# Optimization experiments

Measured on AMD Instinct MI355X. Metric: run time of the kernel, lower is better.

Reference implementation:

```python
import jax, jax.numpy as jnp
import numpy as np
import math

B, L, D, H, FF = 8, 1024, 1024, 16, 4096
DT = D // H  # d_tensor per head
EPS = 1e-12


def _layernorm(x, gamma, beta):
    # Faithful: unbiased std (ddof=1), divide by (std + eps)
    mean = jnp.mean(x, axis=-1, keepdims=True)
    std = jnp.std(x, axis=-1, keepdims=True, ddof=1)
    return gamma * ((x - mean) / (std + EPS)) + beta


def setup_inputs() -> dict:
    key = jax.random.key(0)
    ks = jax.random.split(key, 16)
    sc = 1.0 / math.sqrt(D)
    inp = {
        "x": jax.random.normal(ks[0], (B, L, D), jnp.float32),
        "s_mask": jnp.ones((B, 1, L, L), jnp.int32),
        "wq": jax.random.normal(ks[1], (D, D), jnp.float32) * sc,
        "bq": jnp.zeros((D,), jnp.float32),
        "wk": jax.random.normal(ks[2], (D, D), jnp.float32) * sc,
        "bk": jnp.zeros((D,), jnp.float32),
        "wv": jax.random.normal(ks[3], (D, D), jnp.float32) * sc,
        "bv": jnp.zeros((D,), jnp.float32),
        "wc": jax.random.normal(ks[4], (D, D), jnp.float32) * sc,
        "bc": jnp.zeros((D,), jnp.float32),
        "g1": jnp.ones((D,), jnp.float32),
        "be1": jnp.zeros((D,), jnp.float32),
        "w1": jax.random.normal(ks[5], (D, FF), jnp.float32) * sc,
        "b1": jnp.zeros((FF,), jnp.float32),
        "w2": jax.random.normal(ks[6], (FF, D), jnp.float32) / math.sqrt(FF),
        "b2": jnp.zeros((D,), jnp.float32),
        "g2": jnp.ones((D,), jnp.float32),
        "be2": jnp.zeros((D,), jnp.float32),
    }
    return inp


def reference(x, s_mask, wq, bq, wk, bk, wv, bv, wc, bc, g1, be1, w1, b1, w2, b2, g2, be2):
    _x = x
    q = x @ wq + bq
    k = x @ wk + bk
    v = x @ wv + bv
    # Faithful quirk: split() is a VIEW/reshape [B,L,D] -> [B,H,L,DT], not a transpose-based head split.
    q = q.reshape(B, H, L, DT)
    k = k.reshape(B, H, L, DT)
    v = v.reshape(B, H, L, DT)
    # Faithful quirk: k_t is a reshape to [B,H,DT,L], not a transpose.
    k_t = k.reshape(B, H, DT, L)
    score = jnp.einsum('bhld,bhdm->bhlm', q, k_t) / math.sqrt(DT)
    # Faithful quirk: masked_fill value is -1e-12 (not -inf)
    score = jnp.where(s_mask == 0, jnp.float32(-EPS), score)
    # Faithful quirk: nn.Softmax() with dim=None on 4D tensor -> softmax over dim=1 (head axis)
    score = jax.nn.softmax(score, axis=1)
    out = jnp.einsum('bhlm,bhmd->bhld', score, v)
    out = out.reshape(B, L, D)
    out = out @ wc + bc
    x = _layernorm(out + _x, g1, be1)
    # dropout1: identity at inference
    _x = x
    h = jax.nn.relu(x @ w1 + b1)  # FFN dropout also identity at inference
    h = h @ w2 + b2
    x = _layernorm(h + _x, g2, be2)
    return x
```

## Files before the change

### kernel.cpp

```cpp
#include <hip/hip_runtime.h>
#include <stdint.h>

typedef unsigned short u16;
typedef __attribute__((ext_vector_type(8))) short sx8;
typedef __attribute__((ext_vector_type(4))) float fx4;

__device__ __forceinline__ float bf2f(u16 u) {
    union { unsigned i; float f; } v; v.i = ((unsigned)u) << 16; return v.f;
}
__device__ __forceinline__ u16 f2bf(float f) {
    union { float f; unsigned i; } v; v.f = f;
    return (u16)((v.i + 0x7FFFu + ((v.i >> 16) & 1u)) >> 16);
}
#define MFMA(a, b, c) __builtin_amdgcn_mfma_f32_16x16x32_bf16((a), (b), (c), 0, 0, 0)

#define GLDS(gp, lp) \
    __builtin_amdgcn_global_load_lds((const __attribute__((address_space(1))) void*)(gp), \
                                     (__attribute__((address_space(3))) void*)(lp), 16, 0, 0)

template<int BN>
__global__ __launch_bounds__(256) void gemm_bt(
    const u16* __restrict__ A, long sA, int ldA,
    const u16* __restrict__ BT, long sBT, int ldBT,
    u16* __restrict__ C, long sC, int ldC,
    int K,
    const u16* __restrict__ bias, int bz,
    const void* __restrict__ resid, int residF32, long rofs,
    float scale, int relu)
{
    constexpr int BK = 32;
    constexpr int TM = 4;
    constexpr int TN = BN / 32;
    constexpr int AI = 2;
    constexpr int BI = BN / 64;

    __shared__ __align__(16) u16 As[128 * BK];
    __shared__ __align__(16) u16 Bs[BN * BK];

    const int tid  = threadIdx.x;
    const int w    = tid >> 6;
    const int lane = tid & 63;
    const int quad = lane >> 4;
    const int n16  = lane & 15;
    const int wrow = w >> 1, wcol = w & 1;
    const int m0 = blockIdx.y * 128, n0 = blockIdx.x * BN;
    const long z = blockIdx.z;
    A  += z * sA;
    BT += z * sBT;
    C  += z * sC;

    fx4 acc[TM][TN] = {};

    for (int k0 = 0; k0 < K; k0 += BK) {
        #pragma unroll
        for (int i = 0; i < AI; ++i) {
            unsigned base = (unsigned)(w * AI + i) * 1024u;
            unsigned off  = base + (unsigned)lane * 16u;
            unsigned row  = off >> 6;
            unsigned col  = (off & 63u) >> 1;
            GLDS(A + (long)(m0 + row) * ldA + k0 + col, (char*)As + base);
        }
        #pragma unroll
        for (int i = 0; i < BI; ++i) {
            unsigned base = (unsigned)(w * BI + i) * 1024u;
            unsigned off  = base + (unsigned)lane * 16u;
            unsigned row  = off >> 6;
            unsigned col  = (off & 63u) >> 1;
            GLDS(BT + (long)(n0 + row) * ldBT + k0 + col, (char*)Bs + base);
        }
        __syncthreads();

        sx8 af[TM], bfr[TN];
        #pragma unroll
        for (int r = 0; r < TM; ++r)
            af[r] = *(const sx8*)&As[(wrow * 64 + r * 16 + n16) * BK + quad * 8];
        #pragma unroll
        for (int c = 0; c < TN; ++c)
            bfr[c] = *(const sx8*)&Bs[(wcol * (TN * 16) + c * 16 + n16) * BK + quad * 8];
        #pragma unroll
        for (int r = 0; r < TM; ++r)
            #pragma unroll
            for (int c = 0; c < TN; ++c)
                acc[r][c] = MFMA(af[r], bfr[c], acc[r][c]);
        __syncthreads();
    }

    #pragma unroll
    for (int r = 0; r < TM; ++r) {
        int row = m0 + wrow * 64 + r * 16 + quad * 4;
        #pragma unroll
        for (int c = 0; c < TN; ++c) {
            int col = n0 + wcol * (TN * 16) + c * 16 + n16;
            float bv = bias ? bf2f(bias[bz * (int)z + col]) : 0.f;
            #pragma unroll
            for (int g = 0; g < 4; ++g) {
                long idx = (long)(row + g) * ldC + col;
                float xv = acc[r][c][g] * scale + bv;
                if (resid)
                    xv += residF32 ? ((const float*)resid)[rofs + idx]
                                   : bf2f(((const u16*)resid)[rofs + idx]);
                if (relu) xv = fmaxf(xv, 0.f);
                C[idx] = f2bf(xv);
            }
        }
    }
}

__global__ __launch_bounds__(256, 2) void attn_fused(
    const u16* __restrict__ qb, const u16* __restrict__ kt,
    const u16* __restrict__ vt, const int* __restrict__ mask,
    u16* __restrict__ ao)
{
    constexpr int LM = 136;
    constexpr int SH = 16 * LM;
    __shared__ u16 Ss[16 * SH];

    const int tid = threadIdx.x, w = tid >> 6, lane = tid & 63;
    const int quad = lane >> 4, n16 = lane & 15;
    const int l0 = blockIdx.x * 16;
    const long bo = (long)blockIdx.y * 1048576;

    sx8 qf[4][2];
    #pragma unroll
    for (int i = 0; i < 4; ++i) {
        const u16* qp = qb + bo + (w * 4 + i) * 65536 + (l0 + n16) * 64 + quad * 8;
        qf[i][0] = *(const sx8*)qp;
        qf[i][1] = *(const sx8*)(qp + 32);
    }

    fx4 of[4][4] = {};

    for (int mt = 0; mt < 8; ++mt) {
        const int m0 = mt * 128;
        #pragma unroll
        for (int i = 0; i < 4; ++i) {
            const int h = w * 4 + i;
            const u16* kp = kt + bo + h * 65536 + (long)m0 * 64;
            #pragma unroll
            for (int nt = 0; nt < 8; ++nt) {
                const u16* kr = kp + (nt * 16 + n16) * 64 + quad * 8;
                fx4 s = {};
                s = MFMA(qf[i][0], *(const sx8*)kr, s);
                s = MFMA(qf[i][1], *(const sx8*)(kr + 32), s);
                #pragma unroll
                for (int r = 0; r < 4; ++r)
                    Ss[h * SH + (quad * 4 + r) * LM + nt * 16 + n16] = f2bf(s[r] * 0.125f);
            }
        }
        __syncthreads();
        #pragma unroll
        for (int j = 0; j < 4; ++j) {
            const int p = tid + 256 * j;
            const int l = p >> 6, mp = (p & 63) * 2;
            const int2 mk = *(const int2*)&mask[bo + (long)(l0 + l) * 1024 + m0 + mp];
            u16* col = &Ss[l * LM + mp];
            float v0[16], v1[16], mx0 = -1e30f, mx1 = -1e30f;
            #pragma unroll
            for (int h = 0; h < 16; ++h) {
                unsigned pr = *(const unsigned*)&col[h * SH];
                float a = (mk.x == 0) ? -1e-12f : bf2f((u16)(pr & 0xffff));
                float b = (mk.y == 0) ? -1e-12f : bf2f((u16)(pr >> 16));
                v0[h] = a; v1[h] = b;
                mx0 = fmaxf(mx0, a); mx1 = fmaxf(mx1, b);
            }
            float s0 = 0.f, s1 = 0.f;
            #pragma unroll
            for (int h = 0; h < 16; ++h) {
                v0[h] = __expf(v0[h] - mx0); s0 += v0[h];
                v1[h] = __expf(v1[h] - mx1); s1 += v1[h];
            }
            const float i0 = 1.f / s0, i1 = 1.f / s1;
            #pragma unroll
            for (int h = 0; h < 16; ++h)
                *(unsigned*)&col[h * SH] =
                    (unsigned)f2bf(v0[h] * i0) | ((unsigned)f2bf(v1[h] * i1) << 16);
        }
        __syncthreads();
        #pragma unroll
        for (int i = 0; i < 4; ++i) {
            const int h = w * 4 + i;
            const u16* sp = &Ss[h * SH + n16 * LM];
            sx8 af[4];
            #pragma unroll
            for (int ks = 0; ks < 4; ++ks)
                af[ks] = *(const sx8*)(sp + ks * 32 + quad * 8);
            const u16* vp = vt + bo + h * 65536 + (long)n16 * 1024 + m0 + quad * 8;
            #pragma unroll
            for (int dt = 0; dt < 4; ++dt)
                #pragma unroll
                for (int ks = 0; ks < 4; ++ks)
                    of[i][dt] = MFMA(af[ks], *(const sx8*)(vp + dt * 16384 + ks * 32), of[i][dt]);
        }
        __syncthreads();
    }

    #pragma unroll
    for (int i = 0; i < 4; ++i) {
        const int h = w * 4 + i;
        #pragma unroll
        for (int dt = 0; dt < 4; ++dt)
            #pragma unroll
            for (int r = 0; r < 4; ++r)
                ao[bo + h * 65536 + (long)(l0 + quad * 4 + r) * 64 + dt * 16 + n16]
                    = f2bf(of[i][dt][r]);
    }
}

__global__ __launch_bounds__(256) void convert_f2b(
    const float* __restrict__ in, u16* __restrict__ out)
{
    long i = ((long)blockIdx.x * 256 + threadIdx.x) * 4;
    fx4 v = *(const fx4*)(in + i);
    uint2 o;
    o.x = (unsigned)f2bf(v[0]) | ((unsigned)f2bf(v[1]) << 16);
    o.y = (unsigned)f2bf(v[2]) | ((unsigned)f2bf(v[3]) << 16);
    *(uint2*)(out + i) = o;
}

__global__ __launch_bounds__(256) void transpose_f2b(
    const float* __restrict__ in, u16* __restrict__ out, int R, int C)
{
    __shared__ float t[32][33];
    int c0 = blockIdx.x * 32, r0 = blockIdx.y * 32;
    int tx = threadIdx.x & 31, ty = threadIdx.x >> 5;
    #pragma unroll
    for (int i = 0; i < 4; ++i)
        t[ty + i * 8][tx] = in[(long)(r0 + ty + i * 8) * C + c0 + tx];
    __syncthreads();
    #pragma unroll
    for (int i = 0; i < 4; ++i)
        out[(long)(c0 + ty + i * 8) * R + r0 + tx] = f2bf(t[tx][ty + i * 8]);
}

__global__ __launch_bounds__(256) void transpose_bf(
    const u16* __restrict__ in, u16* __restrict__ out, int R, int C)
{
    __shared__ u16 t[32][33];
    long zoff = (long)blockIdx.z * (long)R * (long)C;
    in += zoff; out += zoff;
    int c0 = blockIdx.x * 32, r0 = blockIdx.y * 32;
    int tx = threadIdx.x & 31, ty = threadIdx.x >> 5;
    #pragma unroll
    for (int i = 0; i < 4; ++i)
        t[ty + i * 8][tx] = in[(long)(r0 + ty + i * 8) * C + c0 + tx];
    __syncthreads();
    #pragma unroll
    for (int i = 0; i < 4; ++i)
        out[(long)(c0 + ty + i * 8) * R + r0 + tx] = t[tx][ty + i * 8];
}

__global__ __launch_bounds__(256) void pack_bias(
    const float* bq, const float* bk, const float* bv, const float* bc,
    const float* b1, const float* b2, u16* __restrict__ out)
{
    int i = blockIdx.x * 256 + threadIdx.x;
    float v;
    if      (i < 1024) v = bq[i];
    else if (i < 2048) v = bk[i - 1024];
    else if (i < 3072) v = bv[i - 2048];
    else if (i < 4096) v = bc[i - 3072];
    else if (i < 8192) v = b1[i - 4096];
    else               v = b2[i - 8192];
    out[i] = f2bf(v);
}

__global__ __launch_bounds__(256) void layernorm_row(
    const u16* __restrict__ in, const float* __restrict__ g,
    const float* __restrict__ be, void* __restrict__ out, int outF32)
{
    int wave = threadIdx.x >> 6, lane = threadIdx.x & 63;
    long row = (long)blockIdx.x * 4 + wave;
    const u16* p = in + row * 1024 + lane * 16;

    float x[16];
    uint4 a = ((const uint4*)p)[0], b = ((const uint4*)p)[1];
    {
        unsigned u;
        u = a.x; x[0] = bf2f(u & 0xffff);  x[1] = bf2f(u >> 16);
        u = a.y; x[2] = bf2f(u & 0xffff);  x[3] = bf2f(u >> 16);
        u = a.z; x[4] = bf2f(u & 0xffff);  x[5] = bf2f(u >> 16);
        u = a.w; x[6] = bf2f(u & 0xffff);  x[7] = bf2f(u >> 16);
        u = b.x; x[8] = bf2f(u & 0xffff);  x[9] = bf2f(u >> 16);
        u = b.y; x[10] = bf2f(u & 0xffff); x[11] = bf2f(u >> 16);
        u = b.z; x[12] = bf2f(u & 0xffff); x[13] = bf2f(u >> 16);
        u = b.w; x[14] = bf2f(u & 0xffff); x[15] = bf2f(u >> 16);
    }
    float s = 0.f, ss = 0.f;
    #pragma unroll
    for (int i = 0; i < 16; ++i) { s += x[i]; ss += x[i] * x[i]; }
    #pragma unroll
    for (int o = 32; o >= 1; o >>= 1) { s += __shfl_down(s, o); ss += __shfl_down(ss, o); }
    s = __shfl(s, 0); ss = __shfl(ss, 0);
    float mean = s * (1.f / 1024.f);
    float var  = fmaxf((ss - 1024.f * mean * mean) * (1.f / 1023.f), 0.f);
    float rinv = 1.f / (sqrtf(var) + 1e-12f);

    int col = lane * 16;
    if (outF32) {
        float* ov = (float*)out + row * 1024 + col;
        #pragma unroll
        for (int i = 0; i < 16; ++i)
            ov[i] = g[col + i] * ((x[i] - mean) * rinv) + be[col + i];
    } else {
        u16* ov = (u16*)out + row * 1024 + col;
        #pragma unroll
        for (int i = 0; i < 16; ++i)
            ov[i] = f2bf(g[col + i] * ((x[i] - mean) * rinv) + be[col + i]);
    }
}

extern "C" void kernel_launch(void* const* d_in, const int* in_sizes, int n_in,
                              void* d_out, int out_size, void* d_ws, size_t ws_size,
                              hipStream_t stream)
{
    const float* xf  = (const float*)d_in[0];
    const int* mask  = (const int*)d_in[1];
    const float* wq = (const float*)d_in[2];  const float* bq = (const float*)d_in[3];
    const float* wk = (const float*)d_in[4];  const float* bk = (const float*)d_in[5];
    const float* wv = (const float*)d_in[6];  const float* bv = (const float*)d_in[7];
    const float* wc = (const float*)d_in[8];  const float* bc = (const float*)d_in[9];
    const float* g1 = (const float*)d_in[10]; const float* be1 = (const float*)d_in[11];
    const float* w1 = (const float*)d_in[12]; const float* b1 = (const float*)d_in[13];
    const float* w2 = (const float*)d_in[14]; const float* b2 = (const float*)d_in[15];
    const float* g2 = (const float*)d_in[16]; const float* be2 = (const float*)d_in[17];

    char* ws = (char*)d_ws;
    const long MB = 1 << 20;
    u16* xb    = (u16*)(ws + 0 * MB);
    u16* wqkvT = (u16*)(ws + 16 * MB);
    u16* wcT   = (u16*)(ws + 22 * MB);
    u16* qb    = (u16*)(ws + 24 * MB);
    u16* kb    = (u16*)(ws + 40 * MB);
    u16* vb    = (u16*)(ws + 56 * MB);
    u16* kt    = (u16*)(ws + 72 * MB);
    u16* vt    = (u16*)(ws + 40 * MB);
    u16* biasp = (u16*)(ws + 96 * MB);
    u16* ao   = xb;
    u16* t0   = qb;
    u16* fh   = kb;
    u16* w1T  = (u16*)(ws + 72 * MB);
    u16* w2T  = (u16*)(ws + 80 * MB);
    u16* pre2 = (u16*)(ws + 88 * MB);

    dim3 blk(256);
    const long M1 = 1048576;

    convert_f2b<<<dim3(8192), blk, 0, stream>>>(xf, xb);
    transpose_f2b<<<dim3(32, 32), blk, 0, stream>>>(wq, wqkvT, 1024, 1024);
    transpose_f2b<<<dim3(32, 32), blk, 0, stream>>>(wk, wqkvT + M1, 1024, 1024);
    transpose_f2b<<<dim3(32, 32), blk, 0, stream>>>(wv, wqkvT + 2 * M1, 1024, 1024);
    transpose_f2b<<<dim3(32, 32), blk, 0, stream>>>(wc, wcT, 1024, 1024);
    pack_bias<<<dim3(36), blk, 0, stream>>>(bq, bk, bv, bc, b1, b2, biasp);

    gemm_bt<128><<<dim3(8, 64, 3), blk, 0, stream>>>(
        xb, 0, 1024, wqkvT, M1, 1024, qb, 8 * M1, 1024, 1024,
        biasp, 1024, nullptr, 0, 0, 1.f, 0);

    transpose_bf<<<dim3(32, 2, 128), blk, 0, stream>>>(kb, kt, 64, 1024);

    transpose_bf<<<dim3(2, 32, 128), blk, 0, stream>>>(vb, vt, 1024, 64);
    attn_fused<<<dim3(64, 8), blk, 0, stream>>>(qb, kt, vt, mask, ao);

    gemm_bt<128><<<dim3(8, 64, 1), blk, 0, stream>>>(
        ao, 0, 1024, wcT, 0, 1024, t0, 0, 1024, 1024,
        biasp + 3072, 0, xf, 1, 0, 1.f, 0);
    layernorm_row<<<dim3(2048), blk, 0, stream>>>(t0, g1, be1, t0, 0);

    transpose_f2b<<<dim3(128, 32), blk, 0, stream>>>(w1, w1T, 1024, 4096);
    transpose_f2b<<<dim3(32, 128), blk, 0, stream>>>(w2, w2T, 4096, 1024);

    for (int c = 0; c < 2; ++c) {
        long r0 = (long)c * 4096 * 1024;
        gemm_bt<128><<<dim3(32, 32, 1), blk, 0, stream>>>(
            t0 + r0, 0, 1024, w1T, 0, 1024, fh, 0, 4096, 1024,
            biasp + 4096, 0, nullptr, 0, 0, 1.f, 1);
        gemm_bt<64><<<dim3(16, 32, 1), blk, 0, stream>>>(
            fh, 0, 4096, w2T, 0, 4096, pre2, 0, 1024, 4096,
            biasp + 8192, 0, t0 + r0, 0, 0, 1.f, 0);
        layernorm_row<<<dim3(1024), blk, 0, stream>>>(
            pre2, g2, be2, (float*)d_out + r0, 1);
    }
}
```

Measured before the change: 956.4 us.

## Split attention key range across two blocks and sum partial outputs

```diff
diff --git a/kernel.cpp b/kernel.cpp
--- a/kernel.cpp
+++ b/kernel.cpp
@@ -106,19 +106,22 @@
     }
 }
 
-__global__ __launch_bounds__(256, 2) void attn_fused(
+__global__ __launch_bounds__(256, 4) void attn_fused(
     const u16* __restrict__ qb, const u16* __restrict__ kt,
     const u16* __restrict__ vt, const int* __restrict__ mask,
-    u16* __restrict__ ao)
-{
-    constexpr int LM = 136;
+    u16* __restrict__ p0, u16* __restrict__ p1)
+{
+    constexpr int MC = 64;
+    constexpr int LM = MC + 8;
     constexpr int SH = 16 * LM;
-    __shared__ u16 Ss[16 * SH];
+    __shared__ __align__(16) u16 Ss[16 * SH];
 
     const int tid = threadIdx.x, w = tid >> 6, lane = tid & 63;
     const int quad = lane >> 4, n16 = lane & 15;
     const int l0 = blockIdx.x * 16;
     const long bo = (long)blockIdx.y * 1048576;
+    const int mbase = blockIdx.z * 512;
+    u16* __restrict__ po = blockIdx.z ? p1 : p0;
 
     sx8 qf[4][2];
     #pragma unroll
@@ -131,27 +134,28 @@
     fx4 of[4][4] = {};
 
     for (int mt = 0; mt < 8; ++mt) {
-        const int m0 = mt * 128;
+        const int m0 = mbase + mt * MC;
         #pragma unroll
         for (int i = 0; i < 4; ++i) {
             const int h = w * 4 + i;
             const u16* kp = kt + bo + h * 65536 + (long)m0 * 64;
             #pragma unroll
-            for (int nt = 0; nt < 8; ++nt) {
+            for (int nt = 0; nt < 4; ++nt) {
                 const u16* kr = kp + (nt * 16 + n16) * 64 + quad * 8;
                 fx4 s = {};
-                s = MFMA(qf[i][0], *(const sx8*)kr, s);
-                s = MFMA(qf[i][1], *(const sx8*)(kr + 32), s);
-                #pragma unroll
-                for (int r = 0; r < 4; ++r)
-                    Ss[h * SH + (quad * 4 + r) * LM + nt * 16 + n16] = f2bf(s[r] * 0.125f);
+                s = MFMA(*(const sx8*)kr,        qf[i][0], s);
+                s = MFMA(*(const sx8*)(kr + 32), qf[i][1], s);
+                uint2 pk;
+                pk.x = (unsigned)f2bf(s[0] * 0.125f) | ((unsigned)f2bf(s[1] * 0.125f) << 16);
+                pk.y = (unsigned)f2bf(s[2] * 0.125f) | ((unsigned)f2bf(s[3] * 0.125f) << 16);
+                *(uint2*)&Ss[h * SH + n16 * LM + nt * 16 + quad * 4] = pk;
             }
         }
         __syncthreads();
         #pragma unroll
-        for (int j = 0; j < 4; ++j) {
+        for (int j = 0; j < 2; ++j) {
             const int p = tid + 256 * j;
-            const int l = p >> 6, mp = (p & 63) * 2;
+            const int l = p >> 5, mp = (p & 31) * 2;
             const int2 mk = *(const int2*)&mask[bo + (long)(l0 + l) * 1024 + m0 + mp];
             u16* col = &Ss[l * LM + mp];
             float v0[16], v1[16], mx0 = -1e30f, mx1 = -1e30f;
@@ -180,16 +184,14 @@
         for (int i = 0; i < 4; ++i) {
             const int h = w * 4 + i;
             const u16* sp = &Ss[h * SH + n16 * LM];
-            sx8 af[4];
-            #pragma unroll
-            for (int ks = 0; ks < 4; ++ks)
-                af[ks] = *(const sx8*)(sp + ks * 32 + quad * 8);
+            sx8 a0 = *(const sx8*)(sp + quad * 8);
+            sx8 a1 = *(const sx8*)(sp + 32 + quad * 8);
             const u16* vp = vt + bo + h * 65536 + (long)n16 * 1024 + m0 + quad * 8;
             #pragma unroll
-            for (int dt = 0; dt < 4; ++dt)
-                #pragma unroll
-                for (int ks = 0; ks < 4; ++ks)
-                    of[i][dt] = MFMA(af[ks], *(const sx8*)(vp + dt * 16384 + ks * 32), of[i][dt]);
+            for (int dt = 0; dt < 4; ++dt) {
+                of[i][dt] = MFMA(a0, *(const sx8*)(vp + dt * 16384),      of[i][dt]);
+                of[i][dt] = MFMA(a1, *(const sx8*)(vp + dt * 16384 + 32), of[i][dt]);
+            }
         }
         __syncthreads();
     }
@@ -201,9 +203,26 @@
         for (int dt = 0; dt < 4; ++dt)
             #pragma unroll
             for (int r = 0; r < 4; ++r)
-                ao[bo + h * 65536 + (long)(l0 + quad * 4 + r) * 64 + dt * 16 + n16]
+                po[bo + h * 65536 + (long)(l0 + quad * 4 + r) * 64 + dt * 16 + n16]
                     = f2bf(of[i][dt][r]);
     }
+}
+
+__global__ __launch_bounds__(256) void add_bf(
+    const u16* __restrict__ a, u16* __restrict__ b)
+{
+    long i = ((long)blockIdx.x * 256 + threadIdx.x) * 8;
+    uint4 x = *(const uint4*)(a + i);
+    uint4 y = *(const uint4*)(b + i);
+    uint4 r;
+    unsigned* xp = (unsigned*)&x; unsigned* yp = (unsigned*)&y; unsigned* rp = (unsigned*)&r;
+    #pragma unroll
+    for (int k = 0; k < 4; ++k) {
+        float lo = bf2f((u16)(xp[k] & 0xffff)) + bf2f((u16)(yp[k] & 0xffff));
+        float hi = bf2f((u16)(xp[k] >> 16))    + bf2f((u16)(yp[k] >> 16));
+        rp[k] = (unsigned)f2bf(lo) | ((unsigned)f2bf(hi) << 16);
+    }
+    *(uint4*)(b + i) = r;
 }
 
 __global__ __launch_bounds__(256) void convert_f2b(
@@ -335,7 +354,9 @@
     u16* kt    = (u16*)(ws + 72 * MB);
     u16* vt    = (u16*)(ws + 40 * MB);
     u16* biasp = (u16*)(ws + 96 * MB);
-    u16* ao   = xb;
+    u16* p0   = xb;
+    u16* p1   = vb;
+    u16* ao   = p1;
     u16* t0   = qb;
     u16* fh   = kb;
     u16* w1T  = (u16*)(ws + 72 * MB);
@@ -359,7 +380,8 @@
     transpose_bf<<<dim3(32, 2, 128), blk, 0, stream>>>(kb, kt, 64, 1024);
 
     transpose_bf<<<dim3(2, 32, 128), blk, 0, stream>>>(vb, vt, 1024, 64);
-    attn_fused<<<dim3(64, 8), blk, 0, stream>>>(qb, kt, vt, mask, ao);
+    attn_fused<<<dim3(64, 8, 2), blk, 0, stream>>>(qb, kt, vt, mask, p0, p1);
+    add_bf<<<dim3(4096), blk, 0, stream>>>(p0, p1);
 
     gemm_bt<128><<<dim3(8, 64, 1), blk, 0, stream>>>(
         ao, 0, 1024, wcT, 0, 1024, t0, 0, 1024, 1024,
```

Measured after the change: 944.6 us. No clear change (-1.2%).
